# Kernel tuning notes

Measured on AMD Instinct MI355X. Metric: run time of the kernel, lower is better.

The kernel has to match this reference:

```python
import jax, jax.numpy as jnp
import numpy as np

H = 2  # num_heads hardcoded in the torch module


def setup_inputs() -> dict:
    key = jax.random.key(0)
    ks = jax.random.split(key, 10)
    B, S, D = 8, 2048, 512
    s = 0.02
    return {
        "rgb": jax.random.normal(ks[0], (B, S, D), jnp.float32),
        "event": jax.random.normal(ks[1], (B, S, D), jnp.float32),
        "w_rgb": jax.random.normal(ks[2], (D, D), jnp.float32) * s,
        "b_rgb": jnp.zeros((D,), jnp.float32),
        "w_event": jax.random.normal(ks[3], (D, D), jnp.float32) * s,
        "b_event": jnp.zeros((D,), jnp.float32),
        "w_in": jax.random.normal(ks[4], (3 * D, D), jnp.float32) * s,   # packed QKV in_proj, torch layout
        "b_in": jnp.zeros((3 * D,), jnp.float32),
        "w_out": jax.random.normal(ks[5], (D, D), jnp.float32) * s,
        "b_out": jnp.zeros((D,), jnp.float32),
    }


def _mha(q_in, kv_in, w_in, b_in, w_out, b_out):
    """torch nn.MultiheadAttention with key==value==kv_in, batch-first math."""
    B, S, D = q_in.shape
    hd = D // H
    q = q_in @ w_in[:D].T + b_in[:D]
    k = kv_in @ w_in[D:2 * D].T + b_in[D:2 * D]
    v = kv_in @ w_in[2 * D:].T + b_in[2 * D:]
    q = q.reshape(B, S, H, hd) * (1.0 / np.sqrt(hd))
    k = k.reshape(B, S, H, hd)
    v = v.reshape(B, S, H, hd)
    scores = jnp.einsum('bqhd,bkhd->bhqk', q, k)          # [B,H,S,S]
    attn = jax.nn.softmax(scores, axis=-1)
    out = jnp.einsum('bhqk,bkhd->bqhd', attn, v).reshape(B, S, D)
    return out @ w_out.T + b_out


def reference(rgb, event, w_rgb, b_rgb, w_event, b_event, w_in, b_in, w_out, b_out):
    rgb_p = rgb @ w_rgb.T + b_rgb
    event_p = event @ w_event.T + b_event
    # same attention weights used for both cross directions
    event_attn = _mha(rgb_p, event_p, w_in, b_in, w_out, b_out)
    rgb_attn = _mha(event_p, rgb_p, w_in, b_in, w_out, b_out)
    gate = jax.nn.sigmoid(jnp.sum(rgb_p * event_p, axis=-1, keepdims=True))
    fused = gate * event_attn + (1.0 - gate) * rgb_attn
    return fused + (rgb_p + event_p) * 0.5
```

## Files before the change

kernel.cpp:

```cpp
#include <hip/hip_runtime.h>
#include <hip/hip_bf16.h>
#include <stdint.h>


typedef __bf16 bf16_t;
typedef __bf16 bf16x8 __attribute__((ext_vector_type(8)));
typedef float f32x4 __attribute__((ext_vector_type(4)));
typedef float f32x16 __attribute__((ext_vector_type(16)));
typedef unsigned int u32;

typedef void gvoid_t __attribute__((address_space(1)));
typedef void svoid_t __attribute__((address_space(3)));

__device__ inline void gload16(const void* g, void* l) {
    __builtin_amdgcn_global_load_lds((gvoid_t*)g, (svoid_t*)l, 16, 0, 0);
}

__device__ inline u32 cvtpk_bf16(float lo, float hi) {
    u32 r;
    asm("v_cvt_pk_bf16_f32 %0, %1, %2" : "=v"(r) : "v"(lo), "v"(hi));
    return r;
}

__device__ inline float exp2v(float x) {
    float r;
    asm("v_exp_f32 %0, %1" : "=v"(r) : "v"(x));
    return r;
}

__global__ __launch_bounds__(256) void f2b_w(const float* __restrict__ s2, bf16_t* __restrict__ d2,
                                             const float* __restrict__ s3, bf16_t* __restrict__ d3,
                                             const float* __restrict__ s4, bf16_t* __restrict__ d4,
                                             const float* __restrict__ s5, bf16_t* __restrict__ d5) {
    int i = blockIdx.x * 256 + threadIdx.x;
    const float* s; bf16_t* d; int off;
    if (i < 32768)       { s = s2; d = d2; off = i; }
    else if (i < 65536)  { s = s3; d = d3; off = i - 32768; }
    else if (i < 163840) { s = s4; d = d4; off = i - 65536; }
    else                 { s = s5; d = d5; off = i - 163840; }
    const float4* p = reinterpret_cast<const float4*>(s) + (size_t)off * 2;
    float4 a = p[0], b = p[1];
    bf16x8 o;
    o[0] = (bf16_t)a.x; o[1] = (bf16_t)a.y; o[2] = (bf16_t)a.z; o[3] = (bf16_t)a.w;
    o[4] = (bf16_t)b.x; o[5] = (bf16_t)b.y; o[6] = (bf16_t)b.z; o[7] = (bf16_t)b.w;
    reinterpret_cast<bf16x8*>(d)[off] = o;
}

template <int MODE>
__global__ __launch_bounds__(256) void gemm_bt(const float* __restrict__ Af,
                                               const float* __restrict__ Af2,
                                               const bf16_t* __restrict__ A,
                                               const bf16_t* __restrict__ A2,
                                               const bf16_t* __restrict__ Bw,
                                               const bf16_t* __restrict__ Bw2,
                                               const float* __restrict__ bias,
                                               const float* __restrict__ bias2,
                                               void* __restrict__ Cout,
                                               void* __restrict__ Cout2,
                                               const bf16_t* __restrict__ r1,
                                               const bf16_t* __restrict__ r2,
                                               const float* __restrict__ gate,
                                               bf16_t* __restrict__ qdst,
                                               bf16_t* __restrict__ kdst,
                                               bf16_t* __restrict__ vdst,
                                               bf16_t* __restrict__ qdst2,
                                               bf16_t* __restrict__ kdst2,
                                               bf16_t* __restrict__ vdst2,
                                               int N, int K) {
    __shared__ __align__(16) bf16_t As[128][64];
    __shared__ __align__(16) bf16_t Bs[128][64];
    const int tid = threadIdx.x, lane = tid & 63, w = tid >> 6;
    const int l16 = lane & 15, l4 = lane >> 4;
    const int wm = w >> 1, wn = w & 1;
    int xt, yt;
    if (MODE == 1) {
        int bid = blockIdx.x;
        int xcd = bid & 7, idx = bid >> 3;
        yt = xcd + 8 * (idx / 12);
        xt = idx % 12;
    } else {
        xt = blockIdx.x; yt = blockIdx.y;
    }
    const bool sec = (MODE != 2) && (yt >= 128);
    const size_t a0 = (size_t)(yt & 127) * 128;
    const size_t b0 = (size_t)xt * 128;
    const bf16_t* Ap = sec ? A2 : A;
    const bf16_t* Bp = sec ? Bw2 : Bw;
    const float* Afp = sec ? Af2 : Af;
    const float* bp = sec ? bias2 : bias;
    f32x4 acc[4][4] = {};
    const int srow = w * 32 + (lane >> 3);
    const int scol = (lane & 7) * 8;
    float g4[4];
    if (MODE == 2) {
#pragma unroll
        for (int i = 0; i < 4; ++i) g4[i] = gate[a0 + srow + i * 8];
    }
    for (int kt = 0; kt < K; kt += 64) {
        __syncthreads();
        if (MODE == 0) {
#pragma unroll
            for (int i = 0; i < 4; ++i) {
                const float4* p = reinterpret_cast<const float4*>(
                    Afp + (a0 + srow + i * 8) * (size_t)K + kt + scol);
                float4 x = p[0], y = p[1];
                bf16x8 o;
                o[0] = (bf16_t)x.x; o[1] = (bf16_t)x.y; o[2] = (bf16_t)x.z; o[3] = (bf16_t)x.w;
                o[4] = (bf16_t)y.x; o[5] = (bf16_t)y.y; o[6] = (bf16_t)y.z; o[7] = (bf16_t)y.w;
                *reinterpret_cast<bf16x8*>(&As[srow + i * 8][scol]) = o;
            }
        } else if (MODE == 2) {
#pragma unroll
            for (int i = 0; i < 4; ++i) {
                size_t ro = (a0 + srow + i * 8) * (size_t)K + kt + scol;
                bf16x8 x = *reinterpret_cast<const bf16x8*>(A + ro);
                bf16x8 y = *reinterpret_cast<const bf16x8*>(A2 + ro);
                bf16x8 o;
#pragma unroll
                for (int j = 0; j < 8; ++j)
                    o[j] = (bf16_t)(g4[i] * (float)x[j] + (1.f - g4[i]) * (float)y[j]);
                *reinterpret_cast<bf16x8*>(&As[srow + i * 8][scol]) = o;
            }
        } else {
#pragma unroll
            for (int i = 0; i < 4; ++i)
                gload16(Ap + (a0 + srow + i * 8) * (size_t)K + kt + scol, &As[w * 32 + i * 8][0]);
        }
#pragma unroll
        for (int i = 0; i < 4; ++i)
            gload16(Bp + (b0 + srow + i * 8) * (size_t)K + kt + scol, &Bs[w * 32 + i * 8][0]);
        __syncthreads();
#pragma unroll
        for (int kk = 0; kk < 2; ++kk) {
            bf16x8 af[4], bfr[4];
#pragma unroll
            for (int mi = 0; mi < 4; ++mi)
                af[mi] = *reinterpret_cast<const bf16x8*>(&As[wm * 64 + mi * 16 + l16][kk * 32 + l4 * 8]);
#pragma unroll
            for (int ni = 0; ni < 4; ++ni)
                bfr[ni] = *reinterpret_cast<const bf16x8*>(&Bs[wn * 64 + ni * 16 + l16][kk * 32 + l4 * 8]);
#pragma unroll
            for (int mi = 0; mi < 4; ++mi)
#pragma unroll
                for (int ni = 0; ni < 4; ++ni)
                    acc[mi][ni] = __builtin_amdgcn_mfma_f32_16x16x32_bf16(af[mi], bfr[ni], acc[mi][ni], 0, 0, 0);
        }
    }
    bf16_t* qd = sec ? qdst2 : qdst;
    bf16_t* kd = sec ? kdst2 : kdst;
    bf16_t* vd = sec ? vdst2 : vdst;
#pragma unroll
    for (int mi = 0; mi < 4; ++mi) {
#pragma unroll
        for (int ni = 0; ni < 4; ++ni) {
            int col = (int)b0 + wn * 64 + ni * 16 + l16;
            float bs = bp[col];
            int row0 = (int)a0 + wm * 64 + mi * 16 + l4 * 4;
            float vv[4];
#pragma unroll
            for (int r = 0; r < 4; ++r) vv[r] = acc[mi][ni][r] + bs;
            if (MODE == 0) {
                bf16_t* Cp = (bf16_t*)(sec ? Cout2 : Cout);
#pragma unroll
                for (int r = 0; r < 4; ++r)
                    Cp[(size_t)(row0 + r) * N + col] = (bf16_t)vv[r];
            } else if (MODE == 2) {
#pragma unroll
                for (int r = 0; r < 4; ++r) {
                    size_t idx = (size_t)(row0 + r) * N + col;
                    ((float*)Cout)[idx] = vv[r] + 0.5f * ((float)r1[idx] + (float)r2[idx]);
                }
            } else {
                if (col < 512) {
#pragma unroll
                    for (int r = 0; r < 4; ++r)
                        qd[(size_t)(row0 + r) * 512 + col] = (bf16_t)(vv[r] * 0.090168440f);
                } else if (col < 1024) {
                    int cc = col - 512, h = cc >> 8, d = cc & 255;
#pragma unroll
                    for (int r = 0; r < 4; ++r) {
                        int row = row0 + r;
                        int bh = (row >> 11) * 2 + h, seq = row & 2047;
                        kd[((size_t)(bh * 64 + (seq >> 5))) * 8192 + (d >> 3) * 256 +
                           (seq & 31) * 8 + (d & 7)] = (bf16_t)vv[r];
                    }
                } else {
                    int cc = col - 1024, h = cc >> 8, d = cc & 255;
                    int bh = (row0 >> 11) * 2 + h, seq = row0 & 2047;
                    size_t idx = ((size_t)(bh * 64 + (seq >> 5))) * 8192 +
                                 ((seq >> 3) & 3) * 2048 + d * 8 + (seq & 7);
                    union { bf16_t h4[4]; uint2 u8; } pk;
#pragma unroll
                    for (int r = 0; r < 4; ++r) pk.h4[r] = (bf16_t)vv[r];
                    *reinterpret_cast<uint2*>(&vd[idx]) = pk.u8;
                }
            }
        }
    }
}

__global__ __launch_bounds__(256) void gate_kernel(const bf16_t* __restrict__ rp,
                                                   const bf16_t* __restrict__ ep,
                                                   float* __restrict__ gate) {
    int row = blockIdx.x * 4 + (threadIdx.x >> 6);
    int lane = threadIdx.x & 63;
    bf16x8 a = reinterpret_cast<const bf16x8*>(rp + (size_t)row * 512)[lane];
    bf16x8 b = reinterpret_cast<const bf16x8*>(ep + (size_t)row * 512)[lane];
    float s = 0.f;
#pragma unroll
    for (int j = 0; j < 8; ++j) s += (float)a[j] * (float)b[j];
#pragma unroll
    for (int off = 32; off; off >>= 1) s += __shfl_xor(s, off, 64);
    if (lane == 0) gate[row] = 1.f / (1.f + __expf(-s));
}

__global__ __launch_bounds__(256, 2) void attn_kernel(const bf16_t* __restrict__ qbr,
                                                      const bf16_t* __restrict__ qbe,
                                                      const bf16_t* __restrict__ kbr,
                                                      const bf16_t* __restrict__ kbe,
                                                      const bf16_t* __restrict__ vbr,
                                                      const bf16_t* __restrict__ vbe,
                                                      bf16_t* __restrict__ out0,
                                                      bf16_t* __restrict__ out1) {
    __shared__ __align__(16) bf16_t smem[32768];
    const int bid = blockIdx.x;
    const int qb = bid >> 5;
    const int combo = bid & 31;
    const int dir = combo >> 4;
    const int bh = combo & 15;
    const int b = bh >> 1, h = bh & 1;
    const bf16_t* Qb = dir ? qbe : qbr;
    const bf16_t* Kc = dir ? kbr : kbe;
    const bf16_t* Vc = dir ? vbr : vbe;
    bf16_t* osrc = dir ? out1 : out0;
    const int tid = threadIdx.x;
    const int w = tid >> 6, l = tid & 63;
    const int l31 = l & 31, hi = l >> 5;
    const int q0w = qb * 128 + w * 32;

    const bf16_t* qp = Qb + ((size_t)(b * 2048 + q0w + l31)) * 512 + h * 256 + hi * 8;
    bf16x8 qf[16];
#pragma unroll
    for (int dch = 0; dch < 16; ++dch)
        qf[dch] = *reinterpret_cast<const bf16x8*>(qp + dch * 16);

    f32x16 O[8] = {};
    f32x16 st;
    float mrun = -1e30f, lrun = 0.f;
    union PA { u32 uw[4]; bf16x8 v; } pa0, pa1;

    const bf16_t* kq = Kc + (size_t)bh * 524288 + (w * 2048 + l * 8);
    const bf16_t* vq = Vc + (size_t)bh * 524288 + (w * 2048 + l * 8);

#define STAGE(T, P)                                                    \
    do {                                                               \
        const bf16_t* ks_ = kq + (size_t)(T) * 8192;                   \
        const bf16_t* vs_ = vq + (size_t)(T) * 8192;                   \
        bf16_t* lk_ = &smem[(P) * 8192 + w * 2048];                    \
        bf16_t* lv_ = &smem[16384 + (P) * 8192 + w * 2048];            \
        gload16(ks_, lk_); gload16(ks_ + 512, lk_ + 512);              \
        gload16(ks_ + 1024, lk_ + 1024); gload16(ks_ + 1536, lk_ + 1536); \
        gload16(vs_, lv_); gload16(vs_ + 512, lv_ + 512);              \
        gload16(vs_ + 1024, lv_ + 1024); gload16(vs_ + 1536, lv_ + 1536); \
    } while (0)

    STAGE(0, 0);

    for (int kt2 = 0; kt2 < 64; ++kt2) {
        asm volatile("s_waitcnt vmcnt(0)" ::: "memory");
        __builtin_amdgcn_s_barrier();
        if (kt2 < 63) STAGE(kt2 + 1, (kt2 + 1) & 1);

        const int cb = kt2 & 1;
        const bf16_t* kb = &smem[cb * 8192 + hi * 256 + l31 * 8];
        const bf16_t* vb = &smem[16384 + cb * 8192 + hi * 2048 + l31 * 8];

#pragma unroll
        for (int r = 0; r < 16; ++r) st[r] = 0.f;
        __builtin_amdgcn_s_setprio(1);
#pragma unroll
        for (int dch = 0; dch < 16; ++dch) {
            bf16x8 kf = *reinterpret_cast<const bf16x8*>(kb + dch * 512);
            st = __builtin_amdgcn_mfma_f32_32x32x16_bf16(kf, qf[dch], st, 0, 0, 0);
        }
        __builtin_amdgcn_s_setprio(0);

        float mx = st[0];
#pragma unroll
        for (int r = 1; r < 16; ++r) mx = fmaxf(mx, st[r]);
        mx = fmaxf(mx, __shfl_xor(mx, 32, 64));
        if (__any(mx - mrun > 8.f)) {
            float mnew = fmaxf(mrun, mx);
            float sc = exp2v(mrun - mnew);
            mrun = mnew;
            lrun *= sc;
#pragma unroll
            for (int r = 0; r < 16; ++r) {
                int qr = (r & 3) + 8 * (r >> 2) + 4 * hi;
                float scr = __shfl(sc, qr, 64);
#pragma unroll
                for (int g = 0; g < 8; ++g) O[g][r] *= scr;
            }
        }
        float lsum = 0.f;
        u32 W[8];
#pragma unroll
        for (int m = 0; m < 8; ++m) {
            float plo = exp2v(st[2 * m] - mrun);
            float phi_ = exp2v(st[2 * m + 1] - mrun);
            lsum += plo + phi_;
            W[m] = cvtpk_bf16(plo, phi_);
        }
        lsum += __shfl_xor(lsum, 32, 64);
        lrun += lsum;
        {
            u32 t0 = hi ? W[0] : W[2], t1 = hi ? W[1] : W[3];
            u32 r0 = (u32)__shfl_xor((int)t0, 32, 64);
            u32 r1 = (u32)__shfl_xor((int)t1, 32, 64);
            pa0.uw[0] = hi ? r0 : W[0]; pa0.uw[1] = hi ? r1 : W[1];
            pa0.uw[2] = hi ? W[2] : r0; pa0.uw[3] = hi ? W[3] : r1;
        }
        {
            u32 t0 = hi ? W[4] : W[6], t1 = hi ? W[5] : W[7];
            u32 r0 = (u32)__shfl_xor((int)t0, 32, 64);
            u32 r1 = (u32)__shfl_xor((int)t1, 32, 64);
            pa1.uw[0] = hi ? r0 : W[4]; pa1.uw[1] = hi ? r1 : W[5];
            pa1.uw[2] = hi ? W[6] : r0; pa1.uw[3] = hi ? W[7] : r1;
        }

        __builtin_amdgcn_s_setprio(1);
#pragma unroll
        for (int g = 0; g < 8; ++g) {
            bf16x8 v0 = *reinterpret_cast<const bf16x8*>(vb + g * 256);
            O[g] = __builtin_amdgcn_mfma_f32_32x32x16_bf16(pa0.v, v0, O[g], 0, 0, 0);
        }
#pragma unroll
        for (int g = 0; g < 8; ++g) {
            bf16x8 v1 = *reinterpret_cast<const bf16x8*>(vb + 4096 + g * 256);
            O[g] = __builtin_amdgcn_mfma_f32_32x32x16_bf16(pa1.v, v1, O[g], 0, 0, 0);
        }
        __builtin_amdgcn_s_setprio(0);
    }
#undef STAGE

#pragma unroll
    for (int r = 0; r < 16; ++r) {
        int qr = (r & 3) + 8 * (r >> 2) + 4 * hi;
        float linv = 1.0f / __shfl(lrun, qr, 64);
        size_t rowoff = ((size_t)(b * 2048 + q0w + qr)) * 512 + h * 256 + l31;
#pragma unroll
        for (int g = 0; g < 8; ++g)
            osrc[rowoff + g * 32] = (bf16_t)(O[g][r] * linv);
    }
}

extern "C" void kernel_launch(void* const* d_in, const int* in_sizes, int n_in,
                              void* d_out, int out_size, void* d_ws, size_t ws_size,
                              hipStream_t stream) {
    const float* rgb = (const float*)d_in[0];
    const float* event = (const float*)d_in[1];
    const float* w_rgb = (const float*)d_in[2];
    const float* b_rgb = (const float*)d_in[3];
    const float* w_event = (const float*)d_in[4];
    const float* b_event = (const float*)d_in[5];
    const float* w_in = (const float*)d_in[6];
    const float* b_in = (const float*)d_in[7];
    const float* w_out = (const float*)d_in[8];
    const float* b_out = (const float*)d_in[9];
    float* out = (float*)d_out;

    const size_t MB16 = (size_t)16 * 1024 * 1024;
    char* ws = (char*)d_ws;
    bf16_t* wrgb_bf = (bf16_t*)(ws + 0);
    bf16_t* wevt_bf = (bf16_t*)(ws + 524288);
    bf16_t* wout_bf = (bf16_t*)(ws + 1048576);
    bf16_t* win_bf = (bf16_t*)(ws + 1572864);
    float* gate = (float*)(ws + 3145728);
    bf16_t* bufA = (bf16_t*)(ws + 4194304);
    bf16_t* bufB = (bf16_t*)(ws + 4194304 + MB16);
    bf16_t* rgbp = (bf16_t*)(ws + 4194304 + 2 * MB16);
    bf16_t* evtp = (bf16_t*)(ws + 4194304 + 3 * MB16);
    bf16_t* qbr  = (bf16_t*)(ws + 4194304 + 4 * MB16);
    bf16_t* qbe  = (bf16_t*)(ws + 4194304 + 5 * MB16);
    bf16_t* kbr  = (bf16_t*)(ws + 4194304 + 6 * MB16);
    bf16_t* kbe  = (bf16_t*)(ws + 4194304 + 7 * MB16);
    bf16_t* vbr  = (bf16_t*)(ws + 4194304 + 8 * MB16);
    bf16_t* vbe  = (bf16_t*)(ws + 4194304 + 9 * MB16);

    dim3 blk(256);
    f2b_w<<<768, blk, 0, stream>>>(w_rgb, wrgb_bf, w_event, wevt_bf,
                                   w_in, win_bf, w_out, wout_bf);
    gemm_bt<0><<<dim3(4, 256), blk, 0, stream>>>(rgb, event, nullptr, nullptr,
                                                 wrgb_bf, wevt_bf, b_rgb, b_event,
                                                 rgbp, evtp, nullptr, nullptr, nullptr,
                                                 nullptr, nullptr, nullptr, nullptr, nullptr,
                                                 nullptr, 512, 512);
    gate_kernel<<<4096, blk, 0, stream>>>(rgbp, evtp, gate);
    gemm_bt<1><<<3072, blk, 0, stream>>>(nullptr, nullptr, rgbp, evtp, win_bf, win_bf,
                                         b_in, b_in, nullptr, nullptr, nullptr, nullptr,
                                         nullptr, qbr, kbr, vbr, qbe, kbe, vbe, 1536, 512);
    attn_kernel<<<512, blk, 0, stream>>>(qbr, qbe, kbr, kbe, vbr, vbe, bufA, bufB);
    gemm_bt<2><<<dim3(4, 128), blk, 0, stream>>>(nullptr, nullptr, bufA, bufB, wout_bf, nullptr,
                                                 b_out, nullptr, out, nullptr, rgbp, evtp, gate,
                                                 nullptr, nullptr, nullptr, nullptr, nullptr,
                                                 nullptr, 512, 512);
}
```

Before: 352.5 us.

## Switch attention Q/K/V and probabilities to FP8 with swizzled K layout

The QKV projection epilogue now writes Q, K and V as FP8 instead of bf16, with a new XOR-swizzled K tile layout and a repacked V layout. The attention kernel runs both the QK^T and PV products with FP8 32x32x16 MFMAs, applies the softmax scale after the score MFMA, and packs the softmax probabilities to FP8. This halves the K/V bytes staged through LDS and global memory and uses the higher-throughput FP8 matrix path. The cost is a large loss of precision in the scores and probabilities, which risks exceeding accuracy tolerance.

```diff
diff --git a/kernel.cpp b/kernel.cpp
--- a/kernel.cpp
+++ b/kernel.cpp
@@ -8,24 +8,31 @@
 typedef float f32x4 __attribute__((ext_vector_type(4)));
 typedef float f32x16 __attribute__((ext_vector_type(16)));
 typedef unsigned int u32;
+typedef unsigned char u8;
 
 typedef void gvoid_t __attribute__((address_space(1)));
 typedef void svoid_t __attribute__((address_space(3)));
 
 __device__ inline void gload16(const void* g, void* l) {
     __builtin_amdgcn_global_load_lds((gvoid_t*)g, (svoid_t*)l, 16, 0, 0);
-}
-
-__device__ inline u32 cvtpk_bf16(float lo, float hi) {
-    u32 r;
-    asm("v_cvt_pk_bf16_f32 %0, %1, %2" : "=v"(r) : "v"(lo), "v"(hi));
-    return r;
 }
 
 __device__ inline float exp2v(float x) {
     float r;
     asm("v_exp_f32 %0, %1" : "=v"(r) : "v"(x));
     return r;
+}
+
+template <bool HI>
+__device__ inline u32 pk_fp8(float a, float b, u32 old) {
+    return (u32)__builtin_amdgcn_cvt_pk_fp8_f32(a, b, (int)old, HI);
+}
+__device__ inline u8 to_fp8(float a) { return (u8)(pk_fp8<false>(a, a, 0) & 0xff); }
+__device__ inline long pk64(u32 lo, u32 hi) {
+    return (long)(((unsigned long long)hi << 32) | (unsigned long long)lo);
+}
+__device__ inline f32x16 mfma_fp8(long a, long b, f32x16 c) {
+    return __builtin_amdgcn_mfma_f32_32x32x16_fp8_fp8(a, b, c, 0, 0, 0);
 }
 
 __global__ __launch_bounds__(256) void f2b_w(const float* __restrict__ s2, bf16_t* __restrict__ d2,
@@ -60,12 +67,12 @@
                                                const bf16_t* __restrict__ r1,
                                                const bf16_t* __restrict__ r2,
                                                const float* __restrict__ gate,
-                                               bf16_t* __restrict__ qdst,
-                                               bf16_t* __restrict__ kdst,
-                                               bf16_t* __restrict__ vdst,
-                                               bf16_t* __restrict__ qdst2,
-                                               bf16_t* __restrict__ kdst2,
-                                               bf16_t* __restrict__ vdst2,
+                                               u8* __restrict__ qdst,
+                                               u8* __restrict__ kdst,
+                                               u8* __restrict__ vdst,
+                                               u8* __restrict__ qdst2,
+                                               u8* __restrict__ kdst2,
+                                               u8* __restrict__ vdst2,
                                                int N, int K) {
     __shared__ __align__(16) bf16_t As[128][64];
     __shared__ __align__(16) bf16_t Bs[128][64];
@@ -146,9 +153,9 @@
                     acc[mi][ni] = __builtin_amdgcn_mfma_f32_16x16x32_bf16(af[mi], bfr[ni], acc[mi][ni], 0, 0, 0);
         }
     }
-    bf16_t* qd = sec ? qdst2 : qdst;
-    bf16_t* kd = sec ? kdst2 : kdst;
-    bf16_t* vd = sec ? vdst2 : vdst;
+    u8* qd = sec ? qdst2 : qdst;
+    u8* kd = sec ? kdst2 : kdst;
+    u8* vd = sec ? vdst2 : vdst;
 #pragma unroll
     for (int mi = 0; mi < 4; ++mi) {
 #pragma unroll
@@ -174,25 +181,27 @@
                 if (col < 512) {
 #pragma unroll
                     for (int r = 0; r < 4; ++r)
-                        qd[(size_t)(row0 + r) * 512 + col] = (bf16_t)(vv[r] * 0.090168440f);
+                        qd[(size_t)(row0 + r) * 512 + col] = to_fp8(vv[r]);
                 } else if (col < 1024) {
-                    int cc = col - 512, h = cc >> 8, d = cc & 255;
+                    int cc = col - 512, hh = cc >> 8, d = cc & 255;
+                    int dpart = ((d >> 3) & 1) * 128 + (d >> 4) * 8 + (d & 7);
 #pragma unroll
                     for (int r = 0; r < 4; ++r) {
                         int row = row0 + r;
-                        int bh = (row >> 11) * 2 + h, seq = row & 2047;
-                        kd[((size_t)(bh * 64 + (seq >> 5))) * 8192 + (d >> 3) * 256 +
-                           (seq & 31) * 8 + (d & 7)] = (bf16_t)vv[r];
+                        int bh = (row >> 11) * 2 + hh, seq = row & 2047;
+                        int rr = seq & 31;
+                        u32 boff = (u32)(rr * 256 + dpart) ^ (u32)((rr & 7) << 4);
+                        kd[((size_t)(bh * 64 + (seq >> 5))) * 8192 + boff] = to_fp8(vv[r]);
                     }
                 } else {
-                    int cc = col - 1024, h = cc >> 8, d = cc & 255;
-                    int bh = (row0 >> 11) * 2 + h, seq = row0 & 2047;
-                    size_t idx = ((size_t)(bh * 64 + (seq >> 5))) * 8192 +
-                                 ((seq >> 3) & 3) * 2048 + d * 8 + (seq & 7);
-                    union { bf16_t h4[4]; uint2 u8; } pk;
-#pragma unroll
-                    for (int r = 0; r < 4; ++r) pk.h4[r] = (bf16_t)vv[r];
-                    *reinterpret_cast<uint2*>(&vd[idx]) = pk.u8;
+                    int cc = col - 1024, hh = cc >> 8, d = cc & 255;
+                    int bh = (row0 >> 11) * 2 + hh, seq = row0 & 2047;
+                    int k = seq & 31;
+                    int s = (k >> 4) & 1, hik = (k >> 3) & 1, j0 = k & 7;
+                    u32 wrd = pk_fp8<false>(vv[0], vv[1], 0);
+                    wrd = pk_fp8<true>(vv[2], vv[3], wrd);
+                    *reinterpret_cast<u32*>(vd + ((size_t)(bh * 64 + (seq >> 5))) * 8192 +
+                                            d * 32 + hik * 16 + s * 8 + j0) = wrd;
                 }
             }
         }
@@ -214,76 +223,76 @@
     if (lane == 0) gate[row] = 1.f / (1.f + __expf(-s));
 }
 
-__global__ __launch_bounds__(256, 2) void attn_kernel(const bf16_t* __restrict__ qbr,
-                                                      const bf16_t* __restrict__ qbe,
-                                                      const bf16_t* __restrict__ kbr,
-                                                      const bf16_t* __restrict__ kbe,
-                                                      const bf16_t* __restrict__ vbr,
-                                                      const bf16_t* __restrict__ vbe,
+__global__ __launch_bounds__(256, 2) void attn_kernel(const u8* __restrict__ qbr,
+                                                      const u8* __restrict__ qbe,
+                                                      const u8* __restrict__ kbr,
+                                                      const u8* __restrict__ kbe,
+                                                      const u8* __restrict__ vbr,
+                                                      const u8* __restrict__ vbe,
                                                       bf16_t* __restrict__ out0,
                                                       bf16_t* __restrict__ out1) {
-    __shared__ __align__(16) bf16_t smem[32768];
+    __shared__ __align__(16) u8 smem[32768];
     const int bid = blockIdx.x;
     const int qb = bid >> 5;
     const int combo = bid & 31;
     const int dir = combo >> 4;
     const int bh = combo & 15;
     const int b = bh >> 1, h = bh & 1;
-    const bf16_t* Qb = dir ? qbe : qbr;
-    const bf16_t* Kc = dir ? kbr : kbe;
-    const bf16_t* Vc = dir ? vbr : vbe;
+    const u8* Qb = dir ? qbe : qbr;
+    const u8* Kc = dir ? kbr : kbe;
+    const u8* Vc = dir ? vbr : vbe;
     bf16_t* osrc = dir ? out1 : out0;
     const int tid = threadIdx.x;
     const int w = tid >> 6, l = tid & 63;
     const int l31 = l & 31, hi = l >> 5;
     const int q0w = qb * 128 + w * 32;
 
-    const bf16_t* qp = Qb + ((size_t)(b * 2048 + q0w + l31)) * 512 + h * 256 + hi * 8;
-    bf16x8 qf[16];
+    const u8* qp = Qb + ((size_t)(b * 2048 + q0w + l31)) * 512 + h * 256 + hi * 8;
+    uint2 qf[16];
 #pragma unroll
     for (int dch = 0; dch < 16; ++dch)
-        qf[dch] = *reinterpret_cast<const bf16x8*>(qp + dch * 16);
+        qf[dch] = *reinterpret_cast<const uint2*>(qp + dch * 16);
 
     f32x16 O[8] = {};
-    f32x16 st;
     float mrun = -1e30f, lrun = 0.f;
-    union PA { u32 uw[4]; bf16x8 v; } pa0, pa1;
-
-    const bf16_t* kq = Kc + (size_t)bh * 524288 + (w * 2048 + l * 8);
-    const bf16_t* vq = Vc + (size_t)bh * 524288 + (w * 2048 + l * 8);
-
-#define STAGE(T, P)                                                    \
-    do {                                                               \
-        const bf16_t* ks_ = kq + (size_t)(T) * 8192;                   \
-        const bf16_t* vs_ = vq + (size_t)(T) * 8192;                   \
-        bf16_t* lk_ = &smem[(P) * 8192 + w * 2048];                    \
-        bf16_t* lv_ = &smem[16384 + (P) * 8192 + w * 2048];            \
-        gload16(ks_, lk_); gload16(ks_ + 512, lk_ + 512);              \
-        gload16(ks_ + 1024, lk_ + 1024); gload16(ks_ + 1536, lk_ + 1536); \
-        gload16(vs_, lv_); gload16(vs_ + 512, lv_ + 512);              \
-        gload16(vs_ + 1024, lv_ + 1024); gload16(vs_ + 1536, lv_ + 1536); \
+
+    const u8* kq = Kc + (size_t)bh * 524288 + w * 2048 + l * 16;
+    const u8* vq = Vc + (size_t)bh * 524288 + w * 2048 + l * 16;
+
+#define STAGE(T, P)                                                          \
+    do {                                                                     \
+        const u8* ks_ = kq + (size_t)(T) * 8192;                             \
+        const u8* vs_ = vq + (size_t)(T) * 8192;                             \
+        gload16(ks_, &smem[(P) * 16384 + w * 2048]);                         \
+        gload16(ks_ + 1024, &smem[(P) * 16384 + w * 2048 + 1024]);           \
+        gload16(vs_, &smem[(P) * 16384 + 8192 + w * 2048]);                  \
+        gload16(vs_ + 1024, &smem[(P) * 16384 + 8192 + w * 2048 + 1024]);    \
     } while (0)
 
     STAGE(0, 0);
 
+    const u32 kx = (u32)((l31 & 7) << 4);
     for (int kt2 = 0; kt2 < 64; ++kt2) {
         asm volatile("s_waitcnt vmcnt(0)" ::: "memory");
         __builtin_amdgcn_s_barrier();
         if (kt2 < 63) STAGE(kt2 + 1, (kt2 + 1) & 1);
 
         const int cb = kt2 & 1;
-        const bf16_t* kb = &smem[cb * 8192 + hi * 256 + l31 * 8];
-        const bf16_t* vb = &smem[16384 + cb * 8192 + hi * 2048 + l31 * 8];
-
-#pragma unroll
-        for (int r = 0; r < 16; ++r) st[r] = 0.f;
+        const u8* kbp = &smem[cb * 16384] + l31 * 256 + hi * 128;
+        const u8* vg = &smem[cb * 16384 + 8192] + l31 * 32 + hi * 16;
+
+        f32x16 st = {};
         __builtin_amdgcn_s_setprio(1);
 #pragma unroll
-        for (int dch = 0; dch < 16; ++dch) {
-            bf16x8 kf = *reinterpret_cast<const bf16x8*>(kb + dch * 512);
-            st = __builtin_amdgcn_mfma_f32_32x32x16_bf16(kf, qf[dch], st, 0, 0, 0);
+        for (int m = 0; m < 8; ++m) {
+            uint4 kk = *reinterpret_cast<const uint4*>(kbp + (((u32)(m << 4)) ^ kx));
+            st = mfma_fp8(pk64(kk.x, kk.y), pk64(qf[2 * m].x, qf[2 * m].y), st);
+            st = mfma_fp8(pk64(kk.z, kk.w), pk64(qf[2 * m + 1].x, qf[2 * m + 1].y), st);
         }
         __builtin_amdgcn_s_setprio(0);
+
+#pragma unroll
+        for (int r = 0; r < 16; ++r) st[r] *= 0.090168440f;
 
         float mx = st[0];
 #pragma unroll
@@ -302,42 +311,28 @@
                 for (int g = 0; g < 8; ++g) O[g][r] *= scr;
             }
         }
+        float p_[16];
         float lsum = 0.f;
-        u32 W[8];
-#pragma unroll
-        for (int m = 0; m < 8; ++m) {
-            float plo = exp2v(st[2 * m] - mrun);
-            float phi_ = exp2v(st[2 * m + 1] - mrun);
-            lsum += plo + phi_;
-            W[m] = cvtpk_bf16(plo, phi_);
-        }
+#pragma unroll
+        for (int r = 0; r < 16; ++r) { p_[r] = exp2v(st[r] - mrun); lsum += p_[r]; }
         lsum += __shfl_xor(lsum, 32, 64);
         lrun += lsum;
-        {
-            u32 t0 = hi ? W[0] : W[2], t1 = hi ? W[1] : W[3];
-            u32 r0 = (u32)__shfl_xor((int)t0, 32, 64);
-            u32 r1 = (u32)__shfl_xor((int)t1, 32, 64);
-            pa0.uw[0] = hi ? r0 : W[0]; pa0.uw[1] = hi ? r1 : W[1];
-            pa0.uw[2] = hi ? W[2] : r0; pa0.uw[3] = hi ? W[3] : r1;
-        }
-        {
-            u32 t0 = hi ? W[4] : W[6], t1 = hi ? W[5] : W[7];
-            u32 r0 = (u32)__shfl_xor((int)t0, 32, 64);
-            u32 r1 = (u32)__shfl_xor((int)t1, 32, 64);
-            pa1.uw[0] = hi ? r0 : W[4]; pa1.uw[1] = hi ? r1 : W[5];
-            pa1.uw[2] = hi ? W[6] : r0; pa1.uw[3] = hi ? W[7] : r1;
-        }
+
+        u32 X0 = pk_fp8<false>(p_[0], p_[1], 0);   X0 = pk_fp8<true>(p_[2], p_[3], X0);
+        u32 X1 = pk_fp8<false>(p_[4], p_[5], 0);   X1 = pk_fp8<true>(p_[6], p_[7], X1);
+        u32 X2 = pk_fp8<false>(p_[8], p_[9], 0);   X2 = pk_fp8<true>(p_[10], p_[11], X2);
+        u32 X3 = pk_fp8<false>(p_[12], p_[13], 0); X3 = pk_fp8<true>(p_[14], p_[15], X3);
+        u32 E0 = (u32)__shfl_xor((int)(hi ? X0 : X1), 32, 64);
+        u32 E1 = (u32)__shfl_xor((int)(hi ? X2 : X3), 32, 64);
+        long A0 = pk64(hi ? E0 : X0, hi ? X1 : E0);
+        long A1 = pk64(hi ? E1 : X2, hi ? X3 : E1);
 
         __builtin_amdgcn_s_setprio(1);
 #pragma unroll
         for (int g = 0; g < 8; ++g) {
-            bf16x8 v0 = *reinterpret_cast<const bf16x8*>(vb + g * 256);
-            O[g] = __builtin_amdgcn_mfma_f32_32x32x16_bf16(pa0.v, v0, O[g], 0, 0, 0);
-        }
-#pragma unroll
-        for (int g = 0; g < 8; ++g) {
-            bf16x8 v1 = *reinterpret_cast<const bf16x8*>(vb + 4096 + g * 256);
-            O[g] = __builtin_amdgcn_mfma_f32_32x32x16_bf16(pa1.v, v1, O[g], 0, 0, 0);
+            uint4 v4 = *reinterpret_cast<const uint4*>(vg + g * 1024);
+            O[g] = mfma_fp8(A0, pk64(v4.x, v4.y), O[g]);
+            O[g] = mfma_fp8(A1, pk64(v4.z, v4.w), O[g]);
         }
         __builtin_amdgcn_s_setprio(0);
     }
@@ -380,12 +375,12 @@
     bf16_t* bufB = (bf16_t*)(ws + 4194304 + MB16);
     bf16_t* rgbp = (bf16_t*)(ws + 4194304 + 2 * MB16);
     bf16_t* evtp = (bf16_t*)(ws + 4194304 + 3 * MB16);
-    bf16_t* qbr  = (bf16_t*)(ws + 4194304 + 4 * MB16);
-    bf16_t* qbe  = (bf16_t*)(ws + 4194304 + 5 * MB16);
-    bf16_t* kbr  = (bf16_t*)(ws + 4194304 + 6 * MB16);
-    bf16_t* kbe  = (bf16_t*)(ws + 4194304 + 7 * MB16);
-    bf16_t* vbr  = (bf16_t*)(ws + 4194304 + 8 * MB16);
-    bf16_t* vbe  = (bf16_t*)(ws + 4194304 + 9 * MB16);
+    u8* qbr = (u8*)(ws + 4194304 + 4 * MB16);
+    u8* qbe = (u8*)(ws + 4194304 + 5 * MB16);
+    u8* kbr = (u8*)(ws + 4194304 + 6 * MB16);
+    u8* kbe = (u8*)(ws + 4194304 + 7 * MB16);
+    u8* vbr = (u8*)(ws + 4194304 + 8 * MB16);
+    u8* vbe = (u8*)(ws + 4194304 + 9 * MB16);
 
     dim3 blk(256);
     f2b_w<<<768, blk, 0, stream>>>(w_rgb, wrgb_bf, w_event, wevt_bf,
```

Result: faster. 303.3 us (-14.0%).
